# Optimization experiments

Hardware: AMD Instinct MI355X
Metric: run time of the kernel (lower is better)

Reference implementation:

```python
import jax, jax.numpy as jnp
import numpy as np

EPS = 0.45  # epsilon_probability


def hard_sigmoid(x):
    # keras K.hard_sigmoid: clip(0.2*x + 0.5, 0, 1)
    return jnp.clip(0.2 * x + 0.5, 0.0, 1.0)


def setup_inputs() -> dict:
    key = jax.random.key(0)
    k1, k2, k3, k4 = jax.random.split(key, 4)
    B, T, F, S, M = 64, 128, 1024, 512, 2048
    return {
        "states": jax.random.normal(k1, (B, T, F), jnp.float32),
        "maximum_routes": jax.random.normal(k2, (B, S, F), jnp.float32),
        "memory": jax.random.normal(k3, (M, F), jnp.float32),   # non-trainable state buffer
        "index": jax.random.normal(k4, (M, 1), jnp.float32),    # priority queue index
    }


def _step(carry, xs):
    # One _update call: eager-TF semantics, state mutated sequentially per batch element.
    memory, index = carry            # (M,F), (M,1)
    state, mr = xs                   # (T,F), (S,F)
    s = state[-1]                    # states[:, -1, :] -> (F,)
    r = state[-1, -1]                # cumsum(rewards, axis=0)[:, -1] over a length-1 axis == last reward (scalar)

    comp_q = 0.5 - hard_sigmoid(memory - s)   # (M,F) compatibility vs queue
    comp_sp = 0.5 - hard_sigmoid(mr - s)      # (S,F) compatibility vs space
    cond_q = jnp.any(comp_q >= EPS)
    cond_s = jnp.any(comp_sp >= EPS)

    # ---- queue branch ----
    cq = comp_q[:, -1]                        # (M,)
    mask_q = (cq == cq.max())[:, None]        # (M,1) max_boolean_mask
    mi = jnp.argmax(cq)
    c = comp_q[mi, -1]                        # scalar
    upd_mem_q = memory[mi] * (1.0 - c) + s * c          # (F,)
    upd_idx_q = index[mi] * (1.0 - c) + r * c           # (1,)
    # NOTE: tf.where(mask, source, value) keeps source where mask True, writes value where False
    mem1 = jnp.where(cond_q, jnp.where(mask_q, memory, upd_mem_q[None, :]), memory)
    idx1 = jnp.where(cond_q, jnp.where(mask_q, index, upd_idx_q[None, :]), index)

    # ---- space branch ----
    # comp_sp has a leading size-1 batch axis in the original ((1,S,F)); argmax over that axis is
    # identically 0, so gather(x, zeros(S), axis=0) stacks S copies of x[0]; tf.norm over that axis
    # is sqrt(S)*|x[0]| and reduce_max of repeated rows is the row itself. Applied below.
    S = mr.shape[0]
    comp_s = jnp.sqrt(jnp.float32(S)) * jnp.max(jnp.abs(comp_sp), axis=0)   # (F,)
    upd_mem_s = jnp.max(mr * comp_s + s * (1.0 - comp_s), axis=0)           # (F,)
    upd_idx_s = mr[0, -1] * comp_s[-1] + r * (1.0 - comp_s[-1])             # scalar
    min_mask = idx1 == jnp.max(-idx1)        # (M,1): index == -min(index)  (as written in source)
    mem2 = jnp.where(cond_s, jnp.where(min_mask, upd_mem_s[None, :], mem1), mem1)
    idx2 = jnp.where(cond_s, jnp.where(min_mask, upd_idx_s, idx1), idx1)

    # ---- fallback branch ----
    cond_e = jnp.logical_and(~cond_q, ~cond_s)
    min_mask2 = idx2 == jnp.max(-idx2)
    mem3 = jnp.where(cond_e, jnp.where(min_mask2, s[None, :], mem2), mem2)
    idx3 = jnp.where(cond_e, jnp.where(min_mask2, r, idx2), idx2)

    # ---- emit queue leader ----
    li = jnp.argmax(idx3[:, 0])
    return (mem3, idx3), (mem3[li], idx3[li])


def reference(states, maximum_routes, memory, index):
    (_, _), (leaders, imps) = jax.lax.scan(_step, (memory, index), (states, maximum_routes))
    targets = leaders[:, None, :]       # (B,1,F)
    importances = imps[:, None, :]      # (B,1,1)
    return targets, importances
```

## Files before the change

### kernel.cpp

```cpp
#include <hip/hip_runtime.h>
#include <stdint.h>

#define NB 64
#define NT 128
#define NF 1024
#define NS 512
#define NM 2048
#define MAXNEW 160
#define SQRT_S 22.627417f

__device__ __forceinline__ float comp_of(float x, float s) {
    float d = __fsub_rn(x, s);
    float t = __fadd_rn(__fmul_rn(0.2f, d), 0.5f);
    t = fminf(fmaxf(t, 0.0f), 1.0f);
    return __fsub_rn(0.5f, t);
}

__device__ __forceinline__ unsigned fkey(float x) {
    unsigned u = __float_as_uint(x);
    return (u & 0x80000000u) ? ~u : (u | 0x80000000u);
}
__device__ __forceinline__ float fkeyInv(unsigned k) {
    return (k & 0x80000000u) ? __uint_as_float(k & 0x7fffffffu) : __uint_as_float(~k);
}
__device__ __forceinline__ unsigned long long packKey(float v, int m) {
    return ((unsigned long long)fkey(v) << 32) | (unsigned)(NM - m);
}

__global__ void k_zero(int* condS) {
    if (threadIdx.x < NB) condS[threadIdx.x] = 0;
}

__global__ void k_routes1(const float* __restrict__ mr,
                          float* __restrict__ pMin, float* __restrict__ pMax) {
    int b = blockIdx.x;
    int f = blockIdx.y * 256 + threadIdx.x;
    int seg = blockIdx.z;
    const float* base = mr + (size_t)b * NS * NF + (size_t)seg * (NS / 4) * NF + f;
    float mn0 = base[0],           mx0 = mn0;
    float mn1 = base[NF],          mx1 = mn1;
    float mn2 = base[2 * NF],      mx2 = mn2;
    float mn3 = base[3 * NF],      mx3 = mn3;
    #pragma unroll 4
    for (int s = 4; s < NS / 4; s += 4) {
        float v0 = base[(size_t)s * NF];
        float v1 = base[(size_t)(s + 1) * NF];
        float v2 = base[(size_t)(s + 2) * NF];
        float v3 = base[(size_t)(s + 3) * NF];
        mn0 = fminf(mn0, v0); mx0 = fmaxf(mx0, v0);
        mn1 = fminf(mn1, v1); mx1 = fmaxf(mx1, v1);
        mn2 = fminf(mn2, v2); mx2 = fmaxf(mx2, v2);
        mn3 = fminf(mn3, v3); mx3 = fmaxf(mx3, v3);
    }
    size_t o = ((size_t)seg * NB + b) * NF + f;
    pMin[o] = fminf(fminf(mn0, mn1), fminf(mn2, mn3));
    pMax[o] = fmaxf(fmaxf(mx0, mx1), fmaxf(mx2, mx3));
}

__global__ void k_routes2(const float* __restrict__ pMin, const float* __restrict__ pMax,
                          const float* __restrict__ mr, const float* __restrict__ states,
                          float* __restrict__ UMS, float* __restrict__ updIdxS,
                          int* __restrict__ condS) {
    int b = blockIdx.x;
    int f = blockIdx.y * 256 + threadIdx.x;
    float mn = INFINITY, mx = -INFINITY;
    #pragma unroll
    for (int seg = 0; seg < 4; ++seg) {
        size_t o = ((size_t)seg * NB + b) * NF + f;
        mn = fminf(mn, pMin[o]);
        mx = fmaxf(mx, pMax[o]);
    }
    float sv = states[((size_t)b * NT + NT - 1) * NF + f];
    float compHi = comp_of(mn, sv);
    float compLo = comp_of(mx, sv);
    float maxabs = fmaxf(compHi, -compLo);
    float cs   = __fmul_rn(SQRT_S, maxabs);
    float omcs = __fsub_rn(1.0f, cs);
    UMS[b * NF + f] = __fadd_rn(__fmul_rn(mx, cs), __fmul_rn(sv, omcs));

    __shared__ int anyf;
    if (threadIdx.x == 0) anyf = 0;
    __syncthreads();
    if (compHi >= 0.45f) atomicOr(&anyf, 1);
    __syncthreads();
    if (threadIdx.x == 0 && anyf) atomicOr(&condS[b], 1);

    if (f == NF - 1) {
        float mr0l = mr[(size_t)b * NS * NF + NF - 1];
        updIdxS[b] = __fadd_rn(__fmul_rn(mr0l, cs), __fmul_rn(sv, omcs));
    }
}

__global__ void k_routes(const float* __restrict__ mr, const float* __restrict__ states,
                         float* __restrict__ UMS, float* __restrict__ updIdxS,
                         int* __restrict__ condS) {
    int b = blockIdx.x;
    int f = blockIdx.y * blockDim.x + threadIdx.x;
    const float* base = mr + (size_t)b * NS * NF + f;
    float mn0 = base[0],      mx0 = mn0;
    float mn1 = base[NF],     mx1 = mn1;
    float mn2 = base[2 * NF], mx2 = mn2;
    float mn3 = base[3 * NF], mx3 = mn3;
    #pragma unroll 4
    for (int s = 4; s < NS; s += 4) {
        float v0 = base[(size_t)s * NF];
        float v1 = base[(size_t)(s + 1) * NF];
        float v2 = base[(size_t)(s + 2) * NF];
        float v3 = base[(size_t)(s + 3) * NF];
        mn0 = fminf(mn0, v0); mx0 = fmaxf(mx0, v0);
        mn1 = fminf(mn1, v1); mx1 = fmaxf(mx1, v1);
        mn2 = fminf(mn2, v2); mx2 = fmaxf(mx2, v2);
        mn3 = fminf(mn3, v3); mx3 = fmaxf(mx3, v3);
    }
    float mn = fminf(fminf(mn0, mn1), fminf(mn2, mn3));
    float mx = fmaxf(fmaxf(mx0, mx1), fmaxf(mx2, mx3));
    float sv = states[((size_t)b * NT + NT - 1) * NF + f];
    float compHi = comp_of(mn, sv);
    float compLo = comp_of(mx, sv);
    float maxabs = fmaxf(compHi, -compLo);
    float cs   = __fmul_rn(SQRT_S, maxabs);
    float omcs = __fsub_rn(1.0f, cs);
    UMS[b * NF + f] = __fadd_rn(__fmul_rn(mx, cs), __fmul_rn(sv, omcs));

    __shared__ int anyf;
    if (threadIdx.x == 0) anyf = 0;
    __syncthreads();
    if (compHi >= 0.45f) atomicOr(&anyf, 1);
    __syncthreads();
    if (threadIdx.x == 0 && anyf) atomicOr(&condS[b], 1);

    if (f == NF - 1) {
        float mr0l = mr[(size_t)b * NS * NF + NF - 1];
        updIdxS[b] = __fadd_rn(__fmul_rn(mr0l, cs), __fmul_rn(sv, omcs));
    }
}

__global__ void k_predorig(const float* __restrict__ memory, const float* __restrict__ states,
                           unsigned long long* __restrict__ predOrig) {
    int m = blockIdx.x, t = threadIdx.x;
    const float4* rowp = (const float4*)(memory + (size_t)m * NF);
    float4 v = rowp[t];
    unsigned long long mask = 0ull;
    for (int b = 0; b < NB; ++b) {
        const float4* sp = (const float4*)(states + ((size_t)b * NT + NT - 1) * NF);
        float4 s = sp[t];
        bool p = (comp_of(v.x, s.x) >= 0.45f) | (comp_of(v.y, s.y) >= 0.45f)
               | (comp_of(v.z, s.z) >= 0.45f) | (comp_of(v.w, s.w) >= 0.45f);
        if (p) mask |= (1ull << b);
    }
    __shared__ unsigned long long sm[256];
    sm[t] = mask;
    __syncthreads();
    for (int off = 128; off > 0; off >>= 1) {
        if (t < off) sm[t] |= sm[t + off];
        __syncthreads();
    }
    if (t == 0) predOrig[m] = sm[0];
}

__global__ void __launch_bounds__(256) k_scan(
    const float* __restrict__ states, const float* __restrict__ memory,
    const float* __restrict__ indexIn, const float* __restrict__ UMS,
    const float* __restrict__ updIdxS, const int* __restrict__ condS,
    const unsigned long long* __restrict__ predOrig, float* __restrict__ vecq,
    float* __restrict__ out)
{
    __shared__ uint16_t rowid[NM];
    __shared__ float idxv[NM];
    __shared__ float cqArr[NM];
    __shared__ float memLast[NM];
    __shared__ unsigned long long pOrig[NM];
    __shared__ const float* poolPtr[MAXNEW];
    __shared__ float poolLastN[MAXNEW];
    __shared__ unsigned char liveN[MAXNEW];
    __shared__ unsigned long long redW[4];
    __shared__ float sFsh;
    __shared__ int flagQ;

    int t = threadIdx.x;
    int lane = t & 63, wid = t >> 6;

    for (int m = t; m < NM; m += 256) {
        rowid[m] = (uint16_t)m;
        idxv[m] = indexIn[m];
        memLast[m] = memory[(size_t)m * NF + NF - 1];
        pOrig[m] = predOrig[m];
    }
    int nCnt = 0;

    for (int b = 0; b < NB; ++b) {
        const float* sG = states + ((size_t)b * NT + NT - 1) * NF;
        float4 s4 = *(const float4*)(sG + 4 * t);
        float4 u4 = *(const float4*)(UMS + (size_t)b * NF + 4 * t);
        int   cS    = condS[b];
        float uIdxS = updIdxS[b];

        __syncthreads();
        if (t == 0) flagQ = 0;
        for (int i = t; i < nCnt; i += 256) liveN[i] = 0;
        if (t == 255) sFsh = s4.w;
        __syncthreads();
        float sF = sFsh;
        float r = sF;

        unsigned long long lk1 = 0; bool lp = false;
        #pragma unroll
        for (int k = 0; k < NM / 256; ++k) {
            int m = t + 256 * k;
            int p = rowid[m];
            float last;
            if (p < NM) {
                last = memLast[p];
                if ((pOrig[p] >> b) & 1ull) lp = true;
            } else {
                last = poolLastN[p - NM];
                liveN[p - NM] = 1;
            }
            float c = comp_of(last, sF);
            cqArr[m] = c;
            unsigned long long kk = packKey(c, m);
            if (kk > lk1) lk1 = kk;
        }
        #pragma unroll
        for (int off = 32; off > 0; off >>= 1) {
            unsigned long long o = __shfl_down(lk1, off, 64);
            if (o > lk1) lk1 = o;
        }
        if (lane == 0) redW[wid] = lk1;
        if (lp) atomicOr(&flagQ, 1);
        __syncthreads();
        unsigned long long bk1 = redW[0];
        #pragma unroll
        for (int w = 1; w < 4; ++w) if (redW[w] > bk1) bk1 = redW[w];
        int   mi    = NM - (int)(bk1 & 0xffffffffull);
        float cqmax = fkeyInv((unsigned)(bk1 >> 32));
        bool condQorig = (flagQ != 0);

        if (!condQorig) {
            bool pp = false;
            for (int i = 0; i < nCnt; ++i) {
                if (liveN[i]) {
                    float4 v = *(const float4*)(poolPtr[i] + 4 * t);
                    if (comp_of(v.x, s4.x) >= 0.45f || comp_of(v.y, s4.y) >= 0.45f ||
                        comp_of(v.z, s4.z) >= 0.45f || comp_of(v.w, s4.w) >= 0.45f) pp = true;
                }
            }
            if (pp) atomicOr(&flagQ, 1);
            __syncthreads();
        }
        bool cond_q = (flagQ != 0);

        if (cond_q) {
            int pmi = rowid[mi];
            float idxmi = idxv[mi];
            const float* src = (pmi < NM) ? (memory + (size_t)pmi * NF) : poolPtr[pmi - NM];
            float4 v = *(const float4*)(src + 4 * t);
            float c = cqmax, omc = __fsub_rn(1.0f, c);
            float updIdxQ = __fadd_rn(__fmul_rn(idxmi, omc), __fmul_rn(r, c));
            float4 o;
            o.x = __fadd_rn(__fmul_rn(v.x, omc), __fmul_rn(s4.x, c));
            o.y = __fadd_rn(__fmul_rn(v.y, omc), __fmul_rn(s4.y, c));
            o.z = __fadd_rn(__fmul_rn(v.z, omc), __fmul_rn(s4.z, c));
            o.w = __fadd_rn(__fmul_rn(v.w, omc), __fmul_rn(s4.w, c));
            *(float4*)(vecq + (size_t)b * NF + 4 * t) = o;
            if (t == 255) poolLastN[nCnt] = o.w;
            if (t == 0)   poolPtr[nCnt] = vecq + (size_t)b * NF;
            int nid = NM + nCnt;
            #pragma unroll
            for (int k = 0; k < NM / 256; ++k) {
                int m = t + 256 * k;
                if (!(cqArr[m] == cqmax)) { rowid[m] = (uint16_t)nid; idxv[m] = updIdxQ; }
            }
            nCnt++;
        }
        __syncthreads();

        bool cond_s = (cS != 0);
        bool cond_e = (!cond_q) && (!cond_s);
        if (cond_s || cond_e) {
            unsigned long long lk2 = 0;
            #pragma unroll
            for (int k = 0; k < NM / 256; ++k) {
                int m = t + 256 * k;
                unsigned long long kk = packKey(-idxv[m], m);
                if (kk > lk2) lk2 = kk;
            }
            #pragma unroll
            for (int off = 32; off > 0; off >>= 1) {
                unsigned long long o = __shfl_down(lk2, off, 64);
                if (o > lk2) lk2 = o;
            }
            if (lane == 0) redW[wid] = lk2;
            __syncthreads();
            unsigned long long bk2 = redW[0];
            #pragma unroll
            for (int w = 1; w < 4; ++w) if (redW[w] > bk2) bk2 = redW[w];
            float mxneg = fkeyInv((unsigned)(bk2 >> 32));
            float newIdx = cond_s ? uIdxS : r;
            if (t == 0)   poolPtr[nCnt] = cond_s ? (UMS + (size_t)b * NF) : sG;
            if (t == 255) poolLastN[nCnt] = cond_s ? u4.w : s4.w;
            int sid = NM + nCnt;
            #pragma unroll
            for (int k = 0; k < NM / 256; ++k) {
                int m = t + 256 * k;
                if (idxv[m] == mxneg) { rowid[m] = (uint16_t)sid; idxv[m] = newIdx; }
            }
            nCnt++;
        }
        __syncthreads();

        unsigned long long lk3 = 0;
        #pragma unroll
        for (int k = 0; k < NM / 256; ++k) {
            int m = t + 256 * k;
            unsigned long long kk = packKey(idxv[m], m);
            if (kk > lk3) lk3 = kk;
        }
        #pragma unroll
        for (int off = 32; off > 0; off >>= 1) {
            unsigned long long o = __shfl_down(lk3, off, 64);
            if (o > lk3) lk3 = o;
        }
        if (lane == 0) redW[wid] = lk3;
        __syncthreads();
        unsigned long long bk3 = redW[0];
        #pragma unroll
        for (int w = 1; w < 4; ++w) if (redW[w] > bk3) bk3 = redW[w];
        int   li   = NM - (int)(bk3 & 0xffffffffull);
        float lidx = fkeyInv((unsigned)(bk3 >> 32));
        int pl = rowid[li];
        const float* lvec = (pl < NM) ? (memory + (size_t)pl * NF) : poolPtr[pl - NM];
        float4 o4 = *(const float4*)(lvec + 4 * t);
        *(float4*)(out + (size_t)b * NF + 4 * t) = o4;
        if (t == 0) out[(size_t)NB * NF + b] = lidx;
    }
}

extern "C" void kernel_launch(void* const* d_in, const int* in_sizes, int n_in,
                              void* d_out, int out_size, void* d_ws, size_t ws_size,
                              hipStream_t stream) {
    (void)out_size;
    const float* states  = (const float*)d_in[0];
    const float* mr      = (const float*)d_in[1];
    const float* memory  = (const float*)d_in[2];
    const float* indexIn = (const float*)d_in[3];
    for (int i = 0; i < n_in; ++i) {
        switch (in_sizes[i]) {
            case NB * NT * NF: states  = (const float*)d_in[i]; break;
            case NB * NS * NF: mr      = (const float*)d_in[i]; break;
            case NM * NF:      memory  = (const float*)d_in[i]; break;
            case NM:           indexIn = (const float*)d_in[i]; break;
            default: break;
        }
    }
    float* out = (float*)d_out;

    char* ws = (char*)d_ws;
    float* UMS      = (float*)ws;
    float* updIdxS  = (float*)(ws + 262144);
    int*   condS    = (int*)(ws + 262400);
    unsigned long long* predOrig = (unsigned long long*)(ws + 262656);
    float* vecq     = (float*)(ws + 279040);
    float* pMin     = (float*)(ws + 541184);
    float* pMax     = (float*)(ws + 803328);
    bool twoStage = (ws_size >= 1065472);

    k_zero<<<1, 64, 0, stream>>>(condS);
    if (twoStage) {
        k_routes1<<<dim3(NB, 4, 4), 256, 0, stream>>>(mr, pMin, pMax);
        k_routes2<<<dim3(NB, 4), 256, 0, stream>>>(pMin, pMax, mr, states, UMS, updIdxS, condS);
    } else {
        k_routes<<<dim3(NB, 4), 256, 0, stream>>>(mr, states, UMS, updIdxS, condS);
    }
    k_predorig<<<NM, 256, 0, stream>>>(memory, states, predOrig);
    k_scan<<<1, 256, 0, stream>>>(states, memory, indexIn, UMS, updIdxS, condS, predOrig, vecq, out);
}
```

Baseline: 480.7 us.

## Cache new queue rows in LDS, prefetch next batch, defer output copy

The serial single-block scan now keeps each queue row's last element in shared memory, so it no longer chases row pointers. Recently created pool rows are held in a small LDS slot cache, and the next batch's inputs are prefetched one iteration ahead. Several barriers are removed by using per-batch flag arrays and separate reduction buffers, and the leader-row copy moves into a separate k_out kernel. The routes min/max kernels are rewritten with float4 loads and 8 segments, and the zeroing kernel is replaced by per-block condition partials. The cost is more LDS use, which with cacheRow is around 64KB+, plus extra slot bookkeeping and an extra kernel launch.

```diff
diff --git a/kernel.cpp b/kernel.cpp
--- a/kernel.cpp
+++ b/kernel.cpp
@@ -6,7 +6,8 @@
 #define NF 1024
 #define NS 512
 #define NM 2048
-#define MAXNEW 160
+#define MAXNEW 128
+#define NSLOT 16
 #define SQRT_S 22.627417f
 
 __device__ __forceinline__ float comp_of(float x, float s) {
@@ -27,73 +28,77 @@
     return ((unsigned long long)fkey(v) << 32) | (unsigned)(NM - m);
 }
 
-__global__ void k_zero(int* condS) {
-    if (threadIdx.x < NB) condS[threadIdx.x] = 0;
-}
-
 __global__ void k_routes1(const float* __restrict__ mr,
                           float* __restrict__ pMin, float* __restrict__ pMax) {
-    int b = blockIdx.x;
-    int f = blockIdx.y * 256 + threadIdx.x;
-    int seg = blockIdx.z;
-    const float* base = mr + (size_t)b * NS * NF + (size_t)seg * (NS / 4) * NF + f;
-    float mn0 = base[0],           mx0 = mn0;
-    float mn1 = base[NF],          mx1 = mn1;
-    float mn2 = base[2 * NF],      mx2 = mn2;
-    float mn3 = base[3 * NF],      mx3 = mn3;
+    int b = blockIdx.x, seg = blockIdx.y, t = threadIdx.x;
+    const float* base = mr + ((size_t)b * NS + (size_t)seg * (NS / 8)) * NF + 4 * t;
+    float4 mn = *(const float4*)base, mx = mn;
     #pragma unroll 4
-    for (int s = 4; s < NS / 4; s += 4) {
-        float v0 = base[(size_t)s * NF];
-        float v1 = base[(size_t)(s + 1) * NF];
-        float v2 = base[(size_t)(s + 2) * NF];
-        float v3 = base[(size_t)(s + 3) * NF];
-        mn0 = fminf(mn0, v0); mx0 = fmaxf(mx0, v0);
-        mn1 = fminf(mn1, v1); mx1 = fmaxf(mx1, v1);
-        mn2 = fminf(mn2, v2); mx2 = fmaxf(mx2, v2);
-        mn3 = fminf(mn3, v3); mx3 = fmaxf(mx3, v3);
-    }
-    size_t o = ((size_t)seg * NB + b) * NF + f;
-    pMin[o] = fminf(fminf(mn0, mn1), fminf(mn2, mn3));
-    pMax[o] = fmaxf(fmaxf(mx0, mx1), fmaxf(mx2, mx3));
+    for (int s = 1; s < NS / 8; ++s) {
+        float4 v = *(const float4*)(base + (size_t)s * NF);
+        mn.x = fminf(mn.x, v.x); mx.x = fmaxf(mx.x, v.x);
+        mn.y = fminf(mn.y, v.y); mx.y = fmaxf(mx.y, v.y);
+        mn.z = fminf(mn.z, v.z); mx.z = fmaxf(mx.z, v.z);
+        mn.w = fminf(mn.w, v.w); mx.w = fmaxf(mx.w, v.w);
+    }
+    size_t o = ((size_t)seg * NB + b) * NF + 4 * t;
+    *(float4*)(pMin + o) = mn;
+    *(float4*)(pMax + o) = mx;
 }
 
 __global__ void k_routes2(const float* __restrict__ pMin, const float* __restrict__ pMax,
                           const float* __restrict__ mr, const float* __restrict__ states,
                           float* __restrict__ UMS, float* __restrict__ updIdxS,
-                          int* __restrict__ condS) {
-    int b = blockIdx.x;
-    int f = blockIdx.y * 256 + threadIdx.x;
-    float mn = INFINITY, mx = -INFINITY;
+                          int* __restrict__ condSpart) {
+    int b = blockIdx.x, t = threadIdx.x;
+    float4 mn = make_float4(INFINITY, INFINITY, INFINITY, INFINITY);
+    float4 mx = make_float4(-INFINITY, -INFINITY, -INFINITY, -INFINITY);
     #pragma unroll
-    for (int seg = 0; seg < 4; ++seg) {
-        size_t o = ((size_t)seg * NB + b) * NF + f;
-        mn = fminf(mn, pMin[o]);
-        mx = fmaxf(mx, pMax[o]);
-    }
-    float sv = states[((size_t)b * NT + NT - 1) * NF + f];
-    float compHi = comp_of(mn, sv);
-    float compLo = comp_of(mx, sv);
-    float maxabs = fmaxf(compHi, -compLo);
-    float cs   = __fmul_rn(SQRT_S, maxabs);
-    float omcs = __fsub_rn(1.0f, cs);
-    UMS[b * NF + f] = __fadd_rn(__fmul_rn(mx, cs), __fmul_rn(sv, omcs));
+    for (int seg = 0; seg < 8; ++seg) {
+        size_t o = ((size_t)seg * NB + b) * NF + 4 * t;
+        float4 a = *(const float4*)(pMin + o);
+        float4 c = *(const float4*)(pMax + o);
+        mn.x = fminf(mn.x, a.x); mx.x = fmaxf(mx.x, c.x);
+        mn.y = fminf(mn.y, a.y); mx.y = fmaxf(mx.y, c.y);
+        mn.z = fminf(mn.z, a.z); mx.z = fmaxf(mx.z, c.z);
+        mn.w = fminf(mn.w, a.w); mx.w = fmaxf(mx.w, c.w);
+    }
+    float4 sv = *(const float4*)(states + ((size_t)b * NT + NT - 1) * NF + 4 * t);
+    float4 hi, lo4, cs, om, ums;
+    hi.x = comp_of(mn.x, sv.x); lo4.x = comp_of(mx.x, sv.x);
+    hi.y = comp_of(mn.y, sv.y); lo4.y = comp_of(mx.y, sv.y);
+    hi.z = comp_of(mn.z, sv.z); lo4.z = comp_of(mx.z, sv.z);
+    hi.w = comp_of(mn.w, sv.w); lo4.w = comp_of(mx.w, sv.w);
+    cs.x = __fmul_rn(SQRT_S, fmaxf(hi.x, -lo4.x)); om.x = __fsub_rn(1.0f, cs.x);
+    cs.y = __fmul_rn(SQRT_S, fmaxf(hi.y, -lo4.y)); om.y = __fsub_rn(1.0f, cs.y);
+    cs.z = __fmul_rn(SQRT_S, fmaxf(hi.z, -lo4.z)); om.z = __fsub_rn(1.0f, cs.z);
+    cs.w = __fmul_rn(SQRT_S, fmaxf(hi.w, -lo4.w)); om.w = __fsub_rn(1.0f, cs.w);
+    ums.x = __fadd_rn(__fmul_rn(mx.x, cs.x), __fmul_rn(sv.x, om.x));
+    ums.y = __fadd_rn(__fmul_rn(mx.y, cs.y), __fmul_rn(sv.y, om.y));
+    ums.z = __fadd_rn(__fmul_rn(mx.z, cs.z), __fmul_rn(sv.z, om.z));
+    ums.w = __fadd_rn(__fmul_rn(mx.w, cs.w), __fmul_rn(sv.w, om.w));
+    *(float4*)(UMS + (size_t)b * NF + 4 * t) = ums;
 
     __shared__ int anyf;
-    if (threadIdx.x == 0) anyf = 0;
+    if (t == 0) anyf = 0;
     __syncthreads();
-    if (compHi >= 0.45f) atomicOr(&anyf, 1);
+    if (hi.x >= 0.45f || hi.y >= 0.45f || hi.z >= 0.45f || hi.w >= 0.45f) atomicOr(&anyf, 1);
     __syncthreads();
-    if (threadIdx.x == 0 && anyf) atomicOr(&condS[b], 1);
-
-    if (f == NF - 1) {
+    if (t == 0) {
+        condSpart[4 * b + 0] = anyf;
+        condSpart[4 * b + 1] = 0;
+        condSpart[4 * b + 2] = 0;
+        condSpart[4 * b + 3] = 0;
+    }
+    if (t == 255) {
         float mr0l = mr[(size_t)b * NS * NF + NF - 1];
-        updIdxS[b] = __fadd_rn(__fmul_rn(mr0l, cs), __fmul_rn(sv, omcs));
+        updIdxS[b] = __fadd_rn(__fmul_rn(mr0l, cs.w), __fmul_rn(sv.w, om.w));
     }
 }
 
 __global__ void k_routes(const float* __restrict__ mr, const float* __restrict__ states,
                          float* __restrict__ UMS, float* __restrict__ updIdxS,
-                         int* __restrict__ condS) {
+                         int* __restrict__ condSpart) {
     int b = blockIdx.x;
     int f = blockIdx.y * blockDim.x + threadIdx.x;
     const float* base = mr + (size_t)b * NS * NF + f;
@@ -127,7 +132,7 @@
     __syncthreads();
     if (compHi >= 0.45f) atomicOr(&anyf, 1);
     __syncthreads();
-    if (threadIdx.x == 0 && anyf) atomicOr(&condS[b], 1);
+    if (threadIdx.x == 0) condSpart[4 * b + blockIdx.y] = anyf;
 
     if (f == NF - 1) {
         float mr0l = mr[(size_t)b * NS * NF + NF - 1];
@@ -158,24 +163,32 @@
     if (t == 0) predOrig[m] = sm[0];
 }
 
+__global__ void k_out(const unsigned long long* __restrict__ srcRec, float* __restrict__ out) {
+    int b = blockIdx.x, t = threadIdx.x;
+    const float* src = (const float*)(uintptr_t)srcRec[b];
+    *(float4*)(out + (size_t)b * NF + 4 * t) = *(const float4*)(src + 4 * t);
+}
+
 __global__ void __launch_bounds__(256) k_scan(
     const float* __restrict__ states, const float* __restrict__ memory,
     const float* __restrict__ indexIn, const float* __restrict__ UMS,
-    const float* __restrict__ updIdxS, const int* __restrict__ condS,
+    const float* __restrict__ updIdxS, const int* __restrict__ condSpart,
     const unsigned long long* __restrict__ predOrig, float* __restrict__ vecq,
-    float* __restrict__ out)
+    unsigned long long* __restrict__ srcRec, float* __restrict__ out)
 {
+    __shared__ float cacheRow[NSLOT][NF];
     __shared__ uint16_t rowid[NM];
     __shared__ float idxv[NM];
     __shared__ float cqArr[NM];
-    __shared__ float memLast[NM];
+    __shared__ float curLast[NM];
     __shared__ unsigned long long pOrig[NM];
     __shared__ const float* poolPtr[MAXNEW];
-    __shared__ float poolLastN[MAXNEW];
-    __shared__ unsigned char liveN[MAXNEW];
-    __shared__ unsigned long long redW[4];
-    __shared__ float sFsh;
-    __shared__ int flagQ;
+    __shared__ unsigned char liveStamp[MAXNEW];
+    __shared__ short poolSlot[MAXNEW];
+    __shared__ uint16_t slotPool[NSLOT];
+    __shared__ unsigned long long redA[4], redB[4], redC[4];
+    __shared__ int flagQArr[NB];
+    __shared__ int chosen1, chosen2, liveLoSh;
 
     int t = threadIdx.x;
     int lane = t & 63, wid = t >> 6;
@@ -183,41 +196,45 @@
     for (int m = t; m < NM; m += 256) {
         rowid[m] = (uint16_t)m;
         idxv[m] = indexIn[m];
-        memLast[m] = memory[(size_t)m * NF + NF - 1];
+        curLast[m] = memory[(size_t)m * NF + NF - 1];
         pOrig[m] = predOrig[m];
     }
+    for (int i = t; i < MAXNEW; i += 256) { liveStamp[i] = 0; poolSlot[i] = -1; }
+    for (int i = t; i < NB; i += 256) flagQArr[i] = 0;
+    if (t < NSLOT) slotPool[t] = 0xFFFF;
+    if (t == 0) liveLoSh = 0;
     int nCnt = 0;
 
+    float4 s4c = *(const float4*)(states + ((size_t)(NT - 1)) * NF + 4 * t);
+    float4 u4c = *(const float4*)(UMS + 4 * t);
+    int4   cSc = *(const int4*)(condSpart);
+    float uIdxSc = updIdxS[0];
+    float sLc = states[((size_t)(NT - 1)) * NF + NF - 1];
+    float uLc = UMS[NF - 1];
+
     for (int b = 0; b < NB; ++b) {
+        int bn = (b + 1 < NB) ? b + 1 : b;
+        const float* sGn = states + ((size_t)bn * NT + NT - 1) * NF;
+        float4 s4n = *(const float4*)(sGn + 4 * t);
+        float4 u4n = *(const float4*)(UMS + (size_t)bn * NF + 4 * t);
+        int4   cSn = *(const int4*)(condSpart + 4 * bn);
+        float uIdxSn = updIdxS[bn];
+        float sLn = sGn[NF - 1];
+        float uLn = UMS[(size_t)bn * NF + NF - 1];
+
         const float* sG = states + ((size_t)b * NT + NT - 1) * NF;
-        float4 s4 = *(const float4*)(sG + 4 * t);
-        float4 u4 = *(const float4*)(UMS + (size_t)b * NF + 4 * t);
-        int   cS    = condS[b];
-        float uIdxS = updIdxS[b];
-
-        __syncthreads();
-        if (t == 0) flagQ = 0;
-        for (int i = t; i < nCnt; i += 256) liveN[i] = 0;
-        if (t == 255) sFsh = s4.w;
-        __syncthreads();
-        float sF = sFsh;
-        float r = sF;
+        float sF = sLc, r = sLc;
+        unsigned char stamp = (unsigned char)(b + 1);
 
         unsigned long long lk1 = 0; bool lp = false;
         #pragma unroll
         for (int k = 0; k < NM / 256; ++k) {
             int m = t + 256 * k;
+            float c = comp_of(curLast[m], sF);
+            cqArr[m] = c;
             int p = rowid[m];
-            float last;
-            if (p < NM) {
-                last = memLast[p];
-                if ((pOrig[p] >> b) & 1ull) lp = true;
-            } else {
-                last = poolLastN[p - NM];
-                liveN[p - NM] = 1;
-            }
-            float c = comp_of(last, sF);
-            cqArr[m] = c;
+            if (p < NM) { if ((pOrig[p] >> b) & 1ull) lp = true; }
+            else liveStamp[p - NM] = stamp;
             unsigned long long kk = packKey(c, m);
             if (kk > lk1) lk1 = kk;
         }
@@ -226,58 +243,96 @@
             unsigned long long o = __shfl_down(lk1, off, 64);
             if (o > lk1) lk1 = o;
         }
-        if (lane == 0) redW[wid] = lk1;
-        if (lp) atomicOr(&flagQ, 1);
-        __syncthreads();
-        unsigned long long bk1 = redW[0];
+        if (lane == 0) redA[wid] = lk1;
+        if (lp) atomicOr(&flagQArr[b], 1);
+        __syncthreads();
+        unsigned long long bk1 = redA[0];
         #pragma unroll
-        for (int w = 1; w < 4; ++w) if (redW[w] > bk1) bk1 = redW[w];
+        for (int w = 1; w < 4; ++w) if (redA[w] > bk1) bk1 = redA[w];
         int   mi    = NM - (int)(bk1 & 0xffffffffull);
         float cqmax = fkeyInv((unsigned)(bk1 >> 32));
-        bool condQorig = (flagQ != 0);
-
+        bool condQorig = (flagQArr[b] != 0);
+
+        int lo = liveLoSh;
+        while (lo < nCnt && liveStamp[lo] != stamp) ++lo;
         if (!condQorig) {
             bool pp = false;
-            for (int i = 0; i < nCnt; ++i) {
-                if (liveN[i]) {
-                    float4 v = *(const float4*)(poolPtr[i] + 4 * t);
-                    if (comp_of(v.x, s4.x) >= 0.45f || comp_of(v.y, s4.y) >= 0.45f ||
-                        comp_of(v.z, s4.z) >= 0.45f || comp_of(v.w, s4.w) >= 0.45f) pp = true;
+            for (int i = lo; i < nCnt; ++i) {
+                if (liveStamp[i] == stamp) {
+                    int sl = poolSlot[i];
+                    const float* vp = (sl >= 0) ? &cacheRow[sl][0] : poolPtr[i];
+                    float4 v = *(const float4*)(vp + 4 * t);
+                    if (comp_of(v.x, s4c.x) >= 0.45f || comp_of(v.y, s4c.y) >= 0.45f ||
+                        comp_of(v.z, s4c.z) >= 0.45f || comp_of(v.w, s4c.w) >= 0.45f) pp = true;
                 }
             }
-            if (pp) atomicOr(&flagQ, 1);
-            __syncthreads();
-        }
-        bool cond_q = (flagQ != 0);
+            if (pp) atomicOr(&flagQArr[b], 1);
+        }
+        if (t == 0) {
+            liveLoSh = lo;
+            int c1 = -1, c2 = -1;
+            for (int s2 = 0; s2 < NSLOT; ++s2) {
+                int id = slotPool[s2];
+                bool fr = (id == 0xFFFF) || (liveStamp[id] != stamp);
+                if (fr) { if (c1 < 0) c1 = s2; else { c2 = s2; break; } }
+            }
+            chosen1 = c1; chosen2 = c2;
+        }
+        __syncthreads();
+        bool cond_q = (flagQArr[b] != 0);
 
         if (cond_q) {
+            int nid = nCnt;
             int pmi = rowid[mi];
-            float idxmi = idxv[mi];
-            const float* src = (pmi < NM) ? (memory + (size_t)pmi * NF) : poolPtr[pmi - NM];
-            float4 v = *(const float4*)(src + 4 * t);
+            float idxmi   = idxv[mi];
+            float srcLast = curLast[mi];
             float c = cqmax, omc = __fsub_rn(1.0f, c);
             float updIdxQ = __fadd_rn(__fmul_rn(idxmi, omc), __fmul_rn(r, c));
+            float oLast   = __fadd_rn(__fmul_rn(srcLast, omc), __fmul_rn(sF, c));
+            float4 v;
+            if (pmi < NM) {
+                v = *(const float4*)(memory + (size_t)pmi * NF + 4 * t);
+            } else {
+                int sl = poolSlot[pmi - NM];
+                const float* sp = (sl >= 0) ? &cacheRow[sl][0] : poolPtr[pmi - NM];
+                v = *(const float4*)(sp + 4 * t);
+            }
             float4 o;
-            o.x = __fadd_rn(__fmul_rn(v.x, omc), __fmul_rn(s4.x, c));
-            o.y = __fadd_rn(__fmul_rn(v.y, omc), __fmul_rn(s4.y, c));
-            o.z = __fadd_rn(__fmul_rn(v.z, omc), __fmul_rn(s4.z, c));
-            o.w = __fadd_rn(__fmul_rn(v.w, omc), __fmul_rn(s4.w, c));
+            o.x = __fadd_rn(__fmul_rn(v.x, omc), __fmul_rn(s4c.x, c));
+            o.y = __fadd_rn(__fmul_rn(v.y, omc), __fmul_rn(s4c.y, c));
+            o.z = __fadd_rn(__fmul_rn(v.z, omc), __fmul_rn(s4c.z, c));
+            o.w = __fadd_rn(__fmul_rn(v.w, omc), __fmul_rn(s4c.w, c));
             *(float4*)(vecq + (size_t)b * NF + 4 * t) = o;
-            if (t == 255) poolLastN[nCnt] = o.w;
-            if (t == 0)   poolPtr[nCnt] = vecq + (size_t)b * NF;
-            int nid = NM + nCnt;
+            int sl1 = chosen1;
+            if (sl1 >= 0) *(float4*)(&cacheRow[sl1][4 * t]) = o;
+            if (t == 0) {
+                poolPtr[nid] = vecq + (size_t)b * NF;
+                liveStamp[nid] = stamp;
+                if (sl1 >= 0) {
+                    int old = slotPool[sl1];
+                    if (old != 0xFFFF) poolSlot[old] = -1;
+                    slotPool[sl1] = (uint16_t)nid;
+                    poolSlot[nid] = (short)sl1;
+                } else poolSlot[nid] = -1;
+            }
+            int nidTag = NM + nid;
             #pragma unroll
             for (int k = 0; k < NM / 256; ++k) {
                 int m = t + 256 * k;
-                if (!(cqArr[m] == cqmax)) { rowid[m] = (uint16_t)nid; idxv[m] = updIdxQ; }
+                if (!(cqArr[m] == cqmax)) {
+                    rowid[m] = (uint16_t)nidTag;
+                    idxv[m] = updIdxQ;
+                    curLast[m] = oLast;
+                }
             }
             nCnt++;
         }
         __syncthreads();
 
-        bool cond_s = (cS != 0);
+        bool cond_s = ((cSc.x | cSc.y | cSc.z | cSc.w) != 0);
         bool cond_e = (!cond_q) && (!cond_s);
         if (cond_s || cond_e) {
+            int sid = nCnt;
             unsigned long long lk2 = 0;
             #pragma unroll
             for (int k = 0; k < NM / 256; ++k) {
@@ -290,20 +345,36 @@
                 unsigned long long o = __shfl_down(lk2, off, 64);
                 if (o > lk2) lk2 = o;
             }
-            if (lane == 0) redW[wid] = lk2;
+            if (lane == 0) redB[wid] = lk2;
             __syncthreads();
-            unsigned long long bk2 = redW[0];
-            #pragma unroll
-            for (int w = 1; w < 4; ++w) if (redW[w] > bk2) bk2 = redW[w];
+            unsigned long long bk2 = redB[0];
+            #pragma unroll
+            for (int w = 1; w < 4; ++w) if (redB[w] > bk2) bk2 = redB[w];
             float mxneg = fkeyInv((unsigned)(bk2 >> 32));
-            float newIdx = cond_s ? uIdxS : r;
-            if (t == 0)   poolPtr[nCnt] = cond_s ? (UMS + (size_t)b * NF) : sG;
-            if (t == 255) poolLastN[nCnt] = cond_s ? u4.w : s4.w;
-            int sid = NM + nCnt;
+            float newIdx  = cond_s ? uIdxSc : r;
+            float newLast = cond_s ? uLc : sF;
+            float4 w4 = cond_s ? u4c : s4c;
+            int sl2 = chosen2;
+            if (sl2 >= 0) *(float4*)(&cacheRow[sl2][4 * t]) = w4;
+            if (t == 0) {
+                poolPtr[sid] = cond_s ? (UMS + (size_t)b * NF) : sG;
+                liveStamp[sid] = stamp;
+                if (sl2 >= 0) {
+                    int old = slotPool[sl2];
+                    if (old != 0xFFFF) poolSlot[old] = -1;
+                    slotPool[sl2] = (uint16_t)sid;
+                    poolSlot[sid] = (short)sl2;
+                } else poolSlot[sid] = -1;
+            }
+            int sidTag = NM + sid;
             #pragma unroll
             for (int k = 0; k < NM / 256; ++k) {
                 int m = t + 256 * k;
-                if (idxv[m] == mxneg) { rowid[m] = (uint16_t)sid; idxv[m] = newIdx; }
+                if (idxv[m] == mxneg) {
+                    rowid[m] = (uint16_t)sidTag;
+                    idxv[m] = newIdx;
+                    curLast[m] = newLast;
+                }
             }
             nCnt++;
         }
@@ -321,18 +392,21 @@
             unsigned long long o = __shfl_down(lk3, off, 64);
             if (o > lk3) lk3 = o;
         }
-        if (lane == 0) redW[wid] = lk3;
-        __syncthreads();
-        unsigned long long bk3 = redW[0];
-        #pragma unroll
-        for (int w = 1; w < 4; ++w) if (redW[w] > bk3) bk3 = redW[w];
-        int   li   = NM - (int)(bk3 & 0xffffffffull);
-        float lidx = fkeyInv((unsigned)(bk3 >> 32));
-        int pl = rowid[li];
-        const float* lvec = (pl < NM) ? (memory + (size_t)pl * NF) : poolPtr[pl - NM];
-        float4 o4 = *(const float4*)(lvec + 4 * t);
-        *(float4*)(out + (size_t)b * NF + 4 * t) = o4;
-        if (t == 0) out[(size_t)NB * NF + b] = lidx;
+        if (lane == 0) redC[wid] = lk3;
+        __syncthreads();
+        if (t == 0) {
+            unsigned long long bk3 = redC[0];
+            #pragma unroll
+            for (int w = 1; w < 4; ++w) if (redC[w] > bk3) bk3 = redC[w];
+            int   li   = NM - (int)(bk3 & 0xffffffffull);
+            float lidx = fkeyInv((unsigned)(bk3 >> 32));
+            int pl = rowid[li];
+            const float* lvec = (pl < NM) ? (memory + (size_t)pl * NF) : poolPtr[pl - NM];
+            srcRec[b] = (unsigned long long)(uintptr_t)lvec;
+            out[(size_t)NB * NF + b] = lidx;
+        }
+
+        s4c = s4n; u4c = u4n; cSc = cSn; uIdxSc = uIdxSn; sLc = sLn; uLc = uLn;
     }
 }
 
@@ -358,20 +432,22 @@
     char* ws = (char*)d_ws;
     float* UMS      = (float*)ws;
     float* updIdxS  = (float*)(ws + 262144);
-    int*   condS    = (int*)(ws + 262400);
-    unsigned long long* predOrig = (unsigned long long*)(ws + 262656);
-    float* vecq     = (float*)(ws + 279040);
-    float* pMin     = (float*)(ws + 541184);
-    float* pMax     = (float*)(ws + 803328);
-    bool twoStage = (ws_size >= 1065472);
-
-    k_zero<<<1, 64, 0, stream>>>(condS);
+    int*   condSpart= (int*)(ws + 262400);
+    unsigned long long* predOrig = (unsigned long long*)(ws + 263424);
+    float* vecq     = (float*)(ws + 279808);
+    unsigned long long* srcRec = (unsigned long long*)(ws + 541952);
+    float* pMin     = (float*)(ws + 542464);
+    float* pMax     = (float*)(ws + 2639616);
+    bool twoStage = (ws_size >= 4736768);
+
     if (twoStage) {
-        k_routes1<<<dim3(NB, 4, 4), 256, 0, stream>>>(mr, pMin, pMax);
-        k_routes2<<<dim3(NB, 4), 256, 0, stream>>>(pMin, pMax, mr, states, UMS, updIdxS, condS);
+        k_routes1<<<dim3(NB, 8), 256, 0, stream>>>(mr, pMin, pMax);
+        k_routes2<<<NB, 256, 0, stream>>>(pMin, pMax, mr, states, UMS, updIdxS, condSpart);
     } else {
-        k_routes<<<dim3(NB, 4), 256, 0, stream>>>(mr, states, UMS, updIdxS, condS);
+        k_routes<<<dim3(NB, 4), 256, 0, stream>>>(mr, states, UMS, updIdxS, condSpart);
     }
     k_predorig<<<NM, 256, 0, stream>>>(memory, states, predOrig);
-    k_scan<<<1, 256, 0, stream>>>(states, memory, indexIn, UMS, updIdxS, condS, predOrig, vecq, out);
-}
+    k_scan<<<1, 256, 0, stream>>>(states, memory, indexIn, UMS, updIdxS, condSpart,
+                                  predOrig, vecq, srcRec, out);
+    k_out<<<NB, 256, 0, stream>>>(srcRec, out);
+}
```

Measured after the change: 541.3 us. 12.6% more time.
